# Kernel optimization log

Hardware: AMD Instinct MI355X
Metric: run time of the kernel (lower is better)

## Reference

```python
import jax, jax.numpy as jnp
import numpy as np

N_NODES = 100000


def gcn_conv(x, W, b, src, tgt, n_nodes):
    """PyG GCNConv: add self-loops, symmetric deg^-1/2 normalization, then aggregate."""
    xw = x @ W  # [N, out]
    # degree including self-loop (edge weights are all 1)
    deg = jnp.zeros((n_nodes,), dtype=x.dtype).at[tgt].add(1.0) + 1.0
    dinv = deg ** -0.5
    norm = dinv[src] * dinv[tgt]  # [E]
    agg = jax.ops.segment_sum(xw[src] * norm[:, None], tgt, num_segments=n_nodes)
    # self-loop contribution: norm_ii = dinv_i^2
    return agg + xw * (dinv ** 2)[:, None] + b


def setup_inputs() -> dict:
    key = jax.random.key(0)
    ks = jax.random.split(key, 9)
    d_in, d_hid, d_out = 128, 128, 64
    x = jax.random.normal(ks[0], (N_NODES, d_in), dtype=jnp.float32)
    edge_index = jax.random.randint(ks[1], (2, 200000), 0, N_NODES)
    pos_edge_index = jax.random.randint(ks[2], (2, 500000), 0, N_NODES)
    s = lambda k, shape, fan: jax.random.normal(k, shape, dtype=jnp.float32) / np.sqrt(fan)
    return {
        "x": x,
        "edge_index": edge_index,
        "pos_edge_index": pos_edge_index,
        "W_init": s(ks[3], (d_in, d_in), d_in),
        "b_init": jnp.zeros((d_in,), dtype=jnp.float32),
        "W1": s(ks[4], (d_in, d_hid), d_in),
        "b1": jnp.zeros((d_hid,), dtype=jnp.float32),
        "W2": s(ks[5], (d_hid, d_out), d_hid),
        "b2": jnp.zeros((d_out,), dtype=jnp.float32),
    }


def reference(x, edge_index, pos_edge_index, W_init, b_init, W1, b1, W2, b2):
    n = x.shape[0]
    src, tgt = pos_edge_index[0], pos_edge_index[1]
    h = x @ W_init + b_init                      # init_linear
    h = gcn_conv(h, W1, b1, src, tgt, n)         # conv1
    h = jax.nn.relu(h)
    h = gcn_conv(h, W2, b2, src, tgt, n)         # conv2
    # edge dot-product scoring (use_bilinear=False)
    logits = jnp.sum(h[edge_index[0]] * h[edge_index[1]], axis=-1)  # [E_pred]
    return logits
```

## Files before the change

kernel.cpp:

```cpp
#include <hip/hip_runtime.h>


typedef __attribute__((ext_vector_type(8))) short short8;
typedef __attribute__((ext_vector_type(4))) float f32x4;

__device__ __forceinline__ ushort f2bf(float v) {
    unsigned u = __float_as_uint(v);
    return (ushort)((u + 0x7FFFu + ((u >> 16) & 1u)) >> 16);
}
__device__ __forceinline__ float bf2f(ushort b) {
    return __uint_as_float(((unsigned)b) << 16);
}
__device__ __forceinline__ float bflo(unsigned u) { return __uint_as_float(u << 16); }
__device__ __forceinline__ float bfhi(unsigned u) { return __uint_as_float(u & 0xFFFF0000u); }
__device__ __forceinline__ unsigned packbf(float x, float y) {
    return (unsigned)f2bf(x) | ((unsigned)f2bf(y) << 16);
}
__device__ __forceinline__ void split2(float v, ushort& h, ushort& l) {
    unsigned u = __float_as_uint(v);
    unsigned hb = (u + 0x7FFFu + ((u >> 16) & 1u)) & 0xFFFF0000u;
    h = (ushort)(hb >> 16);
    l = f2bf(v - __uint_as_float(hb));
}

__global__ void prep_kernel(const float* __restrict__ Wi, const float* __restrict__ W1,
                            const float* __restrict__ W2,
                            ushort* __restrict__ Ti, ushort* __restrict__ T1,
                            ushort* __restrict__ T2, int* __restrict__ zp, int ztot)
{
    int o = blockIdx.x * blockDim.x + threadIdx.x;
    if (o < ztot) zp[o] = 0;
    if (o < 16384) {
        int c = o >> 7, k = o & 127;
        Ti[o] = f2bf(Wi[(size_t)k * 128 + c]);
    } else if (o < 32768) {
        int p = o - 16384;
        int c = p >> 7, k = p & 127;
        T1[p] = f2bf(W1[(size_t)k * 128 + c]);
    } else if (o < 40960) {
        int p = o - 32768;
        int c = p >> 7, k = p & 127;
        T2[p] = f2bf(W2[(size_t)k * 64 + c]);
    }
}

__global__ void hist_kernel(const int* __restrict__ tgt, int* __restrict__ counts, int e) {
    int i = blockIdx.x * blockDim.x + threadIdx.x;
    if (i < e) atomicAdd(&counts[tgt[i]], 1);
}
__global__ __launch_bounds__(256)
void scan1_kernel(const int* __restrict__ counts, int* __restrict__ rowptr,
                  int* __restrict__ bsum, float* __restrict__ dinv, int n)
{
    __shared__ int sdata[256];
    const int t = threadIdx.x;
    const int base = blockIdx.x * 1024 + t * 4;
    int v[4];
#pragma unroll
    for (int i = 0; i < 4; i++) v[i] = (base + i < n) ? counts[base + i] : 0;
#pragma unroll
    for (int i = 0; i < 4; i++)
        if (base + i < n) dinv[base + i] = 1.0f / sqrtf((float)(v[i] + 1));
    int tsum = v[0] + v[1] + v[2] + v[3];
    sdata[t] = tsum;
    __syncthreads();
    for (int off = 1; off < 256; off <<= 1) {
        int x = (t >= off) ? sdata[t - off] : 0;
        __syncthreads();
        if (t >= off) sdata[t] += x;
        __syncthreads();
    }
    if (t == 255) bsum[blockIdx.x] = sdata[255];
    int run = sdata[t] - tsum;
#pragma unroll
    for (int i = 0; i < 4; i++) {
        if (base + i < n) rowptr[base + i] = run;
        run += v[i];
    }
}
__global__ __launch_bounds__(256)
void scan2_kernel(int* __restrict__ bsum, int nb)
{
    __shared__ int sdata[256];
    const int t = threadIdx.x;
    int v = (t < nb) ? bsum[t] : 0;
    sdata[t] = v;
    __syncthreads();
    for (int off = 1; off < 256; off <<= 1) {
        int x = (t >= off) ? sdata[t - off] : 0;
        __syncthreads();
        if (t >= off) sdata[t] += x;
        __syncthreads();
    }
    if (t < nb) bsum[t] = sdata[t] - v;
}
__global__ void scan3_kernel(int* __restrict__ rowptr, const int* __restrict__ bsum,
                             int n, int e_total)
{
    int i = blockIdx.x * blockDim.x + threadIdx.x;
    if (i < n) rowptr[i] += bsum[i >> 10];
    if (i == 0) rowptr[n] = e_total;
}
__global__ void scatter_kernel(const int* __restrict__ src, const int* __restrict__ tgt,
                               const float* __restrict__ dinv, const int* __restrict__ rowptr,
                               int* __restrict__ cursor, int2* __restrict__ ew, int e)
{
    int i = blockIdx.x * blockDim.x + threadIdx.x;
    if (i >= e) return;
    int s = src[i], t = tgt[i];
    int p = rowptr[t] + atomicAdd(&cursor[t], 1);
    ew[p] = make_int2(s, __float_as_int(dinv[s] * dinv[t]));
}

__global__ __launch_bounds__(256)
void fused_gemm01_kernel(const float* __restrict__ x,
                         const ushort* __restrict__ WTi, const ushort* __restrict__ WT1,
                         const float* __restrict__ bias, ushort* __restrict__ xw1, int M)
{
    __shared__ ushort raw[36864];
    ushort (*H0h)[128][8] = (ushort(*)[128][8])raw;
    ushort (*H0l)[128][8] = (ushort(*)[128][8])(raw + 16384);
    ushort (*Bs)[128][8]  = (ushort(*)[128][8])(raw + 32768);

    const int tid = threadIdx.x;
    const int row0 = blockIdx.x * 128;
    const int wv = tid >> 6;
    const int l  = tid & 63;
    const int lr = l & 15;
    const int lk = l >> 4;

    f32x4 acc0[8], acc1[8];
#pragma unroll
    for (int n = 0; n < 8; ++n) {
        acc0[n] = (f32x4){0.f, 0.f, 0.f, 0.f};
        acc1[n] = (f32x4){0.f, 0.f, 0.f, 0.f};
    }

    for (int kk = 0; kk < 128; kk += 32) {
        {
            const int r  = tid >> 1;
            const int kh = tid & 1;
            const int gr = row0 + r;
            float f[16];
            if (gr < M) {
                const float4* p = (const float4*)(x + (size_t)gr * 128 + kk + kh * 16);
                float4 q0 = p[0], q1 = p[1], q2 = p[2], q3 = p[3];
                f[0]=q0.x; f[1]=q0.y; f[2]=q0.z; f[3]=q0.w;
                f[4]=q1.x; f[5]=q1.y; f[6]=q1.z; f[7]=q1.w;
                f[8]=q2.x; f[9]=q2.y; f[10]=q2.z; f[11]=q2.w;
                f[12]=q3.x; f[13]=q3.y; f[14]=q3.z; f[15]=q3.w;
            } else {
#pragma unroll
                for (int j = 0; j < 16; j++) f[j] = 0.f;
            }
#pragma unroll
            for (int uu = 0; uu < 2; ++uu) {
                short8 hv, lv;
#pragma unroll
                for (int j = 0; j < 8; ++j) {
                    ushort h, lo;
                    split2(f[8 * uu + j], h, lo);
                    hv[j] = (short)h; lv[j] = (short)lo;
                }
                *(short8*)&H0h[2 * kh + uu][r][0] = hv;
                *(short8*)&H0l[2 * kh + uu][r][0] = lv;
            }
        }
        {
#pragma unroll
            for (int u = 0; u < 2; ++u) {
                const int unit = tid * 2 + u;
                const int c   = unit >> 2;
                const int kgl = unit & 3;
                *(short8*)&Bs[kgl][c][0] = *(const short8*)(WTi + (size_t)c * 128 + kk + 8 * kgl);
            }
        }
        __syncthreads();
        short8 ah0 = *(const short8*)&H0h[lk][wv * 32 + lr][0];
        short8 ah1 = *(const short8*)&H0h[lk][wv * 32 + 16 + lr][0];
        short8 al0 = *(const short8*)&H0l[lk][wv * 32 + lr][0];
        short8 al1 = *(const short8*)&H0l[lk][wv * 32 + 16 + lr][0];
#pragma unroll
        for (int n = 0; n < 8; ++n) {
            short8 bh = *(const short8*)&Bs[lk][n * 16 + lr][0];
            acc0[n] = __builtin_amdgcn_mfma_f32_16x16x32_bf16(bh, ah0, acc0[n], 0, 0, 0);
            acc1[n] = __builtin_amdgcn_mfma_f32_16x16x32_bf16(bh, ah1, acc1[n], 0, 0, 0);
            acc0[n] = __builtin_amdgcn_mfma_f32_16x16x32_bf16(bh, al0, acc0[n], 0, 0, 0);
            acc1[n] = __builtin_amdgcn_mfma_f32_16x16x32_bf16(bh, al1, acc1[n], 0, 0, 0);
        }
        __syncthreads();
    }

#pragma unroll
    for (int n = 0; n < 8; ++n) {
        const float4 b4 = *(const float4*)(bias + n * 16 + 4 * lk);
        const float bb[4] = {b4.x, b4.y, b4.z, b4.w};
        const int ks = 2 * n + (lk >> 1);
        const int jo = (lk & 1) * 4;
#pragma unroll
        for (int half = 0; half < 2; ++half) {
            const int m = wv * 32 + 16 * half + lr;
            uint2 uh, ul;
            unsigned hw[4], lw[4];
#pragma unroll
            for (int r = 0; r < 4; ++r) {
                ushort h, lo;
                split2((half ? acc1[n][r] : acc0[n][r]) + bb[r], h, lo);
                hw[r] = h; lw[r] = lo;
            }
            uh.x = hw[0] | (hw[1] << 16); uh.y = hw[2] | (hw[3] << 16);
            ul.x = lw[0] | (lw[1] << 16); ul.y = lw[2] | (lw[3] << 16);
            *(uint2*)&H0h[ks][m][jo] = uh;
            *(uint2*)&H0l[ks][m][jo] = ul;
        }
    }
    __syncthreads();

#pragma unroll
    for (int n = 0; n < 8; ++n) {
        acc0[n] = (f32x4){0.f, 0.f, 0.f, 0.f};
        acc1[n] = (f32x4){0.f, 0.f, 0.f, 0.f};
    }
    for (int kk = 0; kk < 4; ++kk) {
        {
#pragma unroll
            for (int u = 0; u < 2; ++u) {
                const int unit = tid * 2 + u;
                const int c   = unit >> 2;
                const int kgl = unit & 3;
                *(short8*)&Bs[kgl][c][0] = *(const short8*)(WT1 + (size_t)c * 128 + kk * 32 + 8 * kgl);
            }
        }
        __syncthreads();
        short8 ah0 = *(const short8*)&H0h[kk * 4 + lk][wv * 32 + lr][0];
        short8 ah1 = *(const short8*)&H0h[kk * 4 + lk][wv * 32 + 16 + lr][0];
        short8 al0 = *(const short8*)&H0l[kk * 4 + lk][wv * 32 + lr][0];
        short8 al1 = *(const short8*)&H0l[kk * 4 + lk][wv * 32 + 16 + lr][0];
#pragma unroll
        for (int n = 0; n < 8; ++n) {
            short8 bh = *(const short8*)&Bs[lk][n * 16 + lr][0];
            acc0[n] = __builtin_amdgcn_mfma_f32_16x16x32_bf16(bh, ah0, acc0[n], 0, 0, 0);
            acc1[n] = __builtin_amdgcn_mfma_f32_16x16x32_bf16(bh, ah1, acc1[n], 0, 0, 0);
            acc0[n] = __builtin_amdgcn_mfma_f32_16x16x32_bf16(bh, al0, acc0[n], 0, 0, 0);
            acc1[n] = __builtin_amdgcn_mfma_f32_16x16x32_bf16(bh, al1, acc1[n], 0, 0, 0);
        }
        __syncthreads();
    }

#pragma unroll
    for (int n = 0; n < 8; ++n) {
#pragma unroll
        for (int half = 0; half < 2; ++half) {
            const int m = row0 + wv * 32 + 16 * half + lr;
            if (m < M) {
                uint2 u;
                const f32x4 a = half ? acc1[n] : acc0[n];
                u.x = (unsigned)f2bf(a[0]) | ((unsigned)f2bf(a[1]) << 16);
                u.y = (unsigned)f2bf(a[2]) | ((unsigned)f2bf(a[3]) << 16);
                *(uint2*)(xw1 + (size_t)m * 128 + n * 16 + 4 * lk) = u;
            }
        }
    }
}

__device__ __forceinline__ void tile_add(unsigned* p, float ax, float ay) {
    unsigned old = *p;
    *p = packbf(bflo(old) + ax, bfhi(old) + ay);
}

__global__ __launch_bounds__(256)
void conv1_fused_kernel(const ushort* __restrict__ xw1, const float* __restrict__ dinv,
                        const int* __restrict__ rowptr, const int2* __restrict__ ew,
                        const float* __restrict__ b1, const ushort* __restrict__ WT2,
                        ushort* __restrict__ xw2, int N)
{
    __shared__ ushort tile[16][65][8];
    __shared__ int srp[65];

    const int tid  = threadIdx.x;
    const int n0   = blockIdx.x * 64;
    const int nc   = min(64, N - n0);
    const int wv   = tid >> 6;
    const int lane = tid & 63;

    if (tid <= nc) srp[tid] = rowptr[n0 + tid];

    const float bb0 = b1[2 * lane];
    const float bb1 = b1[2 * lane + 1];
    const int  kg = lane >> 2;
    const int  jj = (2 * lane) & 7;
    unsigned* tbase = (unsigned*)&tile[kg][0][jj];
    for (int r = wv; r < 64; r += 4) {
        float vx = 0.f, vy = 0.f;
        if (r < nc) {
            unsigned u = *(const unsigned*)(xw1 + (size_t)(n0 + r) * 128 + 2 * lane);
            float dt = dinv[n0 + r];
            float cc = dt * dt;
            vx = fmaf(bflo(u), cc, bb0);
            vy = fmaf(bfhi(u), cc, bb1);
        }
        tbase[r * 4] = packbf(vx, vy);
    }
    __syncthreads();

    const int nlo = wv * 16;
    if (nlo < nc) {
        const int nhi = min(nlo + 16, nc);
        const int e0 = srp[0];
        int i = srp[nlo] - e0;
        const int iend = srp[nhi] - e0;
        int cur = nlo;
        int nxt = srp[nlo + 1] - e0;
        float ax = 0.f, ay = 0.f;

        for (; i + 8 <= iend; i += 8) {
            int2 d[8];
#pragma unroll
            for (int u = 0; u < 8; ++u) d[u] = ew[e0 + i + u];
            unsigned v[8];
#pragma unroll
            for (int u = 0; u < 8; ++u)
                v[u] = *(const unsigned*)(xw1 + (size_t)d[u].x * 128 + 2 * lane);
#pragma unroll
            for (int u = 0; u < 8; ++u) {
                const int idx = i + u;
                while (idx >= nxt) {
                    tile_add(tbase + cur * 4, ax, ay);
                    ax = 0.f; ay = 0.f;
                    ++cur;
                    nxt = srp[cur + 1] - e0;
                }
                const float w = __int_as_float(d[u].y);
                ax = fmaf(bflo(v[u]), w, ax);
                ay = fmaf(bfhi(v[u]), w, ay);
            }
        }
        for (; i < iend; ++i) {
            int2 d = ew[e0 + i];
            unsigned v = *(const unsigned*)(xw1 + (size_t)d.x * 128 + 2 * lane);
            while (i >= nxt) {
                tile_add(tbase + cur * 4, ax, ay);
                ax = 0.f; ay = 0.f;
                ++cur;
                nxt = srp[cur + 1] - e0;
            }
            const float w = __int_as_float(d.y);
            ax = fmaf(bflo(v), w, ax);
            ay = fmaf(bfhi(v), w, ay);
        }
        tile_add(tbase + cur * 4, ax, ay);
    }
    __syncthreads();

    const int lr = lane & 15;
    const int lk = lane >> 4;
    f32x4 acc[4];
#pragma unroll
    for (int n = 0; n < 4; ++n) acc[n] = (f32x4){0.f, 0.f, 0.f, 0.f};

    for (int kt = 0; kt < 4; ++kt) {
        short8 ah = *(const short8*)&tile[kt * 4 + lk][wv * 16 + lr][0];
#pragma unroll
        for (int j = 0; j < 8; ++j) {
            ushort vv = (ushort)ah[j];
            ah[j] = (short)((vv & 0x8000u) ? 0 : vv);
        }
#pragma unroll
        for (int n = 0; n < 4; ++n) {
            short8 bh = *(const short8*)(WT2 + (size_t)(n * 16 + lr) * 128 + kt * 32 + lk * 8);
            acc[n] = __builtin_amdgcn_mfma_f32_16x16x32_bf16(bh, ah, acc[n], 0, 0, 0);
        }
    }

    const int ml = wv * 16 + lr;
    if (ml < nc) {
        const size_t m = (size_t)(n0 + ml);
#pragma unroll
        for (int n = 0; n < 4; ++n) {
            uint2 u;
            u.x = (unsigned)f2bf(acc[n][0]) | ((unsigned)f2bf(acc[n][1]) << 16);
            u.y = (unsigned)f2bf(acc[n][2]) | ((unsigned)f2bf(acc[n][3]) << 16);
            *(uint2*)(xw2 + m * 64 + n * 16 + 4 * lk) = u;
        }
    }
}

__global__ __launch_bounds__(256)
void gather2_kernel(const ushort* __restrict__ xw, const float* __restrict__ dinv,
                    const int* __restrict__ rowptr, const int2* __restrict__ ew,
                    const float* __restrict__ bias, ushort* __restrict__ out, int n)
{
    const int node = blockIdx.x * 4 + (threadIdx.x >> 6);
    const int lane = threadIdx.x & 63;
    if (node >= n) return;
    const float dt = dinv[node];
    int j = rowptr[node];
    const int j1 = rowptr[node + 1];

    float acc = fmaf(bf2f(xw[(size_t)node * 64 + lane]), dt * dt, bias[lane]);
    for (; j + 8 <= j1; j += 8) {
        int2 d[8];
#pragma unroll
        for (int u = 0; u < 8; ++u) d[u] = ew[j + u];
        float v[8];
#pragma unroll
        for (int u = 0; u < 8; ++u) v[u] = bf2f(xw[(size_t)d[u].x * 64 + lane]);
#pragma unroll
        for (int u = 0; u < 8; ++u) acc = fmaf(v[u], __int_as_float(d[u].y), acc);
    }
    for (; j < j1; ++j) {
        const int2 p0 = ew[j];
        acc = fmaf(bf2f(xw[(size_t)p0.x * 64 + lane]), __int_as_float(p0.y), acc);
    }
    out[(size_t)node * 64 + lane] = f2bf(acc);
}

__global__ void score_kernel(const ushort* __restrict__ h, const int* __restrict__ ea,
                             const int* __restrict__ eb, float* __restrict__ out, int E)
{
    long long gid = (long long)blockIdx.x * blockDim.x + threadIdx.x;
    int e = (int)(gid >> 3);
    int l = (int)(gid & 7);
    if (e >= E) return;
    int a = ea[e], b = eb[e];
    uint4 ua = *(const uint4*)(h + (size_t)a * 64 + 8 * l);
    uint4 ub = *(const uint4*)(h + (size_t)b * 64 + 8 * l);
    float s;
    s  = __uint_as_float(ua.x << 16)         * __uint_as_float(ub.x << 16);
    s += __uint_as_float(ua.x & 0xFFFF0000u) * __uint_as_float(ub.x & 0xFFFF0000u);
    s += __uint_as_float(ua.y << 16)         * __uint_as_float(ub.y << 16);
    s += __uint_as_float(ua.y & 0xFFFF0000u) * __uint_as_float(ub.y & 0xFFFF0000u);
    s += __uint_as_float(ua.z << 16)         * __uint_as_float(ub.z << 16);
    s += __uint_as_float(ua.z & 0xFFFF0000u) * __uint_as_float(ub.z & 0xFFFF0000u);
    s += __uint_as_float(ua.w << 16)         * __uint_as_float(ub.w << 16);
    s += __uint_as_float(ua.w & 0xFFFF0000u) * __uint_as_float(ub.w & 0xFFFF0000u);
    s += __shfl_xor(s, 4);
    s += __shfl_xor(s, 2);
    s += __shfl_xor(s, 1);
    if (l == 0) out[e] = s;
}

extern "C" void kernel_launch(void* const* d_in, const int* in_sizes, int n_in,
                              void* d_out, int out_size, void* d_ws, size_t ws_size,
                              hipStream_t stream)
{
    const float* x              = (const float*)d_in[0];
    const int*   edge_index     = (const int*)d_in[1];
    const int*   pos_edge_index = (const int*)d_in[2];
    const float* W_init         = (const float*)d_in[3];
    const float* b_init         = (const float*)d_in[4];
    const float* W1             = (const float*)d_in[5];
    const float* b1             = (const float*)d_in[6];
    const float* W2             = (const float*)d_in[7];
    const float* b2             = (const float*)d_in[8];
    float* out = (float*)d_out;

    const int N     = in_sizes[0] / 128;
    const int Epred = in_sizes[1] / 2;
    const int E     = in_sizes[2] / 2;

    const int* src = pos_edge_index;
    const int* tgt = pos_edge_index + E;
    const int* ea  = edge_index;
    const int* eb  = edge_index + Epred;

    int2*   ew   = (int2*)d_ws;
    ushort* regA = (ushort*)(ew + E);
    ushort* regB = regA + (size_t)N * 128;
    float*  dinv = (float*)(regB + (size_t)N * 128);
    int*   counts = (int*)(dinv + N);
    int*   cursor = counts + N;
    int*   rowptr = cursor + N;
    int*   bsum   = rowptr + N + 2;
    ushort* WTi = (ushort*)(((uintptr_t)(bsum + 256) + 15) & ~(uintptr_t)15);
    ushort* WT1 = WTi + 16384;
    ushort* WT2 = WT1 + 16384;

    ushort* xw1 = regA;
    ushort* xw2 = regB;
    ushort* h2  = regB + (size_t)N * 64;

    const int BLK = 256;
    const int nb  = (N + 1023) / 1024;

    prep_kernel<<<(2 * N + BLK - 1) / BLK, BLK, 0, stream>>>(
        W_init, W1, W2, WTi, WT1, WT2, counts, 2 * N);

    hist_kernel<<<(E + BLK - 1) / BLK, BLK, 0, stream>>>(tgt, counts, E);
    scan1_kernel<<<nb, 256, 0, stream>>>(counts, rowptr, bsum, dinv, N);
    scan2_kernel<<<1, 256, 0, stream>>>(bsum, nb);
    scan3_kernel<<<(N + BLK - 1) / BLK, BLK, 0, stream>>>(rowptr, bsum, N, E);
    scatter_kernel<<<(E + BLK - 1) / BLK, BLK, 0, stream>>>(src, tgt, dinv, rowptr, cursor, ew, E);

    fused_gemm01_kernel<<<(N + 127) / 128, BLK, 0, stream>>>(x, WTi, WT1, b_init, xw1, N);

    conv1_fused_kernel<<<(N + 63) / 64, BLK, 0, stream>>>(
        xw1, dinv, rowptr, ew, b1, WT2, xw2, N);

    gather2_kernel<<<(N + 3) / 4, BLK, 0, stream>>>(xw2, dinv, rowptr, ew, b2, h2, N);

    score_kernel<<<((long long)Epred * 8 + BLK - 1) / BLK, BLK, 0, stream>>>(
        h2, ea, eb, out, Epred);
}
```

Measured before the change: 197.2 us.

## Flatten conv2 gather over edge ranges of 16-node groups per wavefront

Replaces the one-wavefront-per-node conv2 aggregation with a kernel where each wavefront walks the flattened CSR edge range of 16 consecutive nodes. Row boundaries are staged in shared memory and results are flushed when the edge index crosses a boundary. With an average of about 5 edges per node, this keeps the 8-wide unrolled loads busy and avoids most of the scalar tail loops. In exchange it adds per-edge boundary checks that can diverge, plus a shared-memory setup and barrier per block.

```diff
diff --git a/kernel.cpp b/kernel.cpp
--- a/kernel.cpp
+++ b/kernel.cpp
@@ -386,19 +386,40 @@
 }
 
 __global__ __launch_bounds__(256)
-void gather2_kernel(const ushort* __restrict__ xw, const float* __restrict__ dinv,
-                    const int* __restrict__ rowptr, const int2* __restrict__ ew,
-                    const float* __restrict__ bias, ushort* __restrict__ out, int n)
-{
-    const int node = blockIdx.x * 4 + (threadIdx.x >> 6);
-    const int lane = threadIdx.x & 63;
-    if (node >= n) return;
-    const float dt = dinv[node];
-    int j = rowptr[node];
-    const int j1 = rowptr[node + 1];
-
-    float acc = fmaf(bf2f(xw[(size_t)node * 64 + lane]), dt * dt, bias[lane]);
-    for (; j + 8 <= j1; j += 8) {
+void gather2_flat_kernel(const ushort* __restrict__ xw, const float* __restrict__ dinv,
+                         const int* __restrict__ rowptr, const int2* __restrict__ ew,
+                         const float* __restrict__ bias, ushort* __restrict__ out, int N)
+{
+    __shared__ int srp[65];
+
+    const int tid  = threadIdx.x;
+    const int n0   = blockIdx.x * 64;
+    const int nc   = min(64, N - n0);
+    const int wv   = tid >> 6;
+    const int lane = tid & 63;
+
+    if (tid <= nc) srp[tid] = rowptr[n0 + tid];
+    __syncthreads();
+
+    const int nlo = wv * 16;
+    if (nlo >= nc) return;
+    const int nhi = min(nlo + 16, nc);
+    const float bl = bias[lane];
+
+    int j = srp[nlo];
+    const int jend = srp[nhi];
+    int cur = nlo;
+    int nxt = srp[nlo + 1];
+    float acc = 0.f;
+
+    auto flush = [&](int c, float a) {
+        const size_t g = (size_t)(n0 + c);
+        const float self = bf2f(xw[g * 64 + lane]);
+        const float dt = dinv[g];
+        out[g * 64 + lane] = f2bf(fmaf(self, dt * dt, a + bl));
+    };
+
+    for (; j + 8 <= jend; j += 8) {
         int2 d[8];
 #pragma unroll
         for (int u = 0; u < 8; ++u) d[u] = ew[j + u];
@@ -406,13 +427,30 @@
 #pragma unroll
         for (int u = 0; u < 8; ++u) v[u] = bf2f(xw[(size_t)d[u].x * 64 + lane]);
 #pragma unroll
-        for (int u = 0; u < 8; ++u) acc = fmaf(v[u], __int_as_float(d[u].y), acc);
-    }
-    for (; j < j1; ++j) {
-        const int2 p0 = ew[j];
-        acc = fmaf(bf2f(xw[(size_t)p0.x * 64 + lane]), __int_as_float(p0.y), acc);
-    }
-    out[(size_t)node * 64 + lane] = f2bf(acc);
+        for (int u = 0; u < 8; ++u) {
+            const int idx = j + u;
+            while (idx >= nxt) {
+                flush(cur, acc);
+                acc = 0.f;
+                ++cur;
+                nxt = srp[cur + 1];
+            }
+            acc = fmaf(v[u], __int_as_float(d[u].y), acc);
+        }
+    }
+    for (; j < jend; ++j) {
+        int2 d = ew[j];
+        float v = bf2f(xw[(size_t)d.x * 64 + lane]);
+        while (j >= nxt) {
+            flush(cur, acc);
+            acc = 0.f;
+            ++cur;
+            nxt = srp[cur + 1];
+        }
+        acc = fmaf(v, __int_as_float(d.y), acc);
+    }
+    flush(cur, acc);
+    for (int c = cur + 1; c < nhi; ++c) flush(c, 0.f);
 }
 
 __global__ void score_kernel(const ushort* __restrict__ h, const int* __restrict__ ea,
@@ -497,7 +535,8 @@
     conv1_fused_kernel<<<(N + 63) / 64, BLK, 0, stream>>>(
         xw1, dinv, rowptr, ew, b1, WT2, xw2, N);
 
-    gather2_kernel<<<(N + 3) / 4, BLK, 0, stream>>>(xw2, dinv, rowptr, ew, b2, h2, N);
+    gather2_flat_kernel<<<(N + 63) / 64, BLK, 0, stream>>>(
+        xw2, dinv, rowptr, ew, b2, h2, N);
 
     score_kernel<<<((long long)Epred * 8 + BLK - 1) / BLK, BLK, 0, stream>>>(
         h2, ea, eb, out, Epred);
```

Result: faster. 175.3 us (-11.1%).
